# Performance work log

Measured on AMD Instinct MI355X. Metric: run time of the kernel, lower is better.

The kernel has to match this reference:

```python
import jax, jax.numpy as jnp
import numpy as np

NUM_HEADS = 12

def _get_rel_pos(q_size, k_size, rel_pos):
    # rel_pos already has shape (2*max(q,k)-1, head_dim) -> no resize needed
    q_coords = jnp.arange(q_size)[:, None] * max(k_size / q_size, 1.0)
    k_coords = jnp.arange(k_size)[None, :] * max(q_size / k_size, 1.0)
    rel = (q_coords - k_coords + (k_size - 1) * max(q_size / k_size, 1.0)).astype(jnp.int32)
    return rel_pos[rel.reshape(-1)].reshape(q_size, k_size, -1)  # (q, k, head_dim)


def setup_inputs() -> dict:
    key = jax.random.key(0)
    ks = jax.random.split(key, 7)
    B, H, W, C = 1, 64, 64, 768
    head_dim = C // NUM_HEADS
    return {
        "x": jax.random.normal(ks[0], (B, H, W, C), jnp.float32),
        "qkv_w": jax.random.normal(ks[1], (C, 3 * C), jnp.float32) * 0.02,
        "qkv_b": jax.random.normal(ks[2], (3 * C,), jnp.float32) * 0.02,
        "rel_pos_h": jax.random.normal(ks[3], (2 * H - 1, head_dim), jnp.float32) * 0.02,
        "rel_pos_w": jax.random.normal(ks[4], (2 * W - 1, head_dim), jnp.float32) * 0.02,
        "proj_w": jax.random.normal(ks[5], (C, C), jnp.float32) * 0.02,
        "proj_b": jax.random.normal(ks[6], (C,), jnp.float32) * 0.02,
    }


def reference(x, qkv_w, qkv_b, rel_pos_h, rel_pos_w, proj_w, proj_b):
    B, H, W, C = x.shape
    nh = NUM_HEADS
    hd = C // nh
    scale = hd ** (-0.5)
    S = H * W

    qkv = x @ qkv_w + qkv_b                              # (B,H,W,3C)
    qkv = qkv.reshape(B, S, 3, nh, hd).transpose(2, 0, 3, 1, 4).reshape(3, B * nh, S, hd)
    q, k, v = qkv[0], qkv[1], qkv[2]                     # (B*nh, S, hd)

    attn = jnp.einsum('bqd,bkd->bqk', q * scale, k)      # (B*nh, S, S)

    rh = _get_rel_pos(H, H, rel_pos_h)                   # (H,H,hd)
    rw = _get_rel_pos(W, W, rel_pos_w)                   # (W,W,hd)
    r_q = q.reshape(B * nh, H, W, hd)
    rel_h = jnp.einsum('bhwc,hkc->bhwk', r_q, rh)        # (B*nh,H,W,H)
    rel_w = jnp.einsum('bhwc,wkc->bhwk', r_q, rw)        # (B*nh,H,W,W)
    attn = (attn.reshape(B * nh, H, W, H, W)
            + rel_h[:, :, :, :, None]
            + rel_w[:, :, :, None, :]).reshape(B * nh, S, S)

    attn = jax.nn.softmax(attn, axis=-1)
    out = jnp.einsum('bqk,bkd->bqd', attn, v)            # (B*nh, S, hd)
    out = out.reshape(B, nh, H, W, hd).transpose(0, 2, 3, 1, 4).reshape(B, H, W, C)
    return out @ proj_w + proj_b
```

## Files before the change

kernel.cpp:

```cpp
#include <hip/hip_runtime.h>
#include <hip/hip_bf16.h>

#define S_TOK 4096
#define CDIM  768
#define N3C   2304
#define NH    12
#define HD    64

#define LOG2E 1.44269504f

typedef __attribute__((ext_vector_type(8))) short short8;
typedef __attribute__((ext_vector_type(4))) short short4v;
typedef __attribute__((ext_vector_type(4))) float float4v;
typedef __attribute__((ext_vector_type(4))) unsigned uint4v;

__device__ __forceinline__ float b2f(short s) {
    return __uint_as_float(((unsigned)(unsigned short)s) << 16);
}
__device__ __forceinline__ short f2b(float f) {
    unsigned u = __float_as_uint(f);
    unsigned r = (u + 0x7FFFu + ((u >> 16) & 1u)) >> 16;
    return (short)r;
}

#if __has_builtin(__builtin_amdgcn_exp2f)
#define EXP2F __builtin_amdgcn_exp2f
#else
#define EXP2F exp2f
#endif

__device__ __forceinline__ unsigned pack_trunc(float a, float b) {
    return __builtin_amdgcn_perm(__float_as_uint(b), __float_as_uint(a), 0x07060302u);
}

__device__ __forceinline__ short8 u4_to_s8(unsigned a, unsigned b, unsigned c, unsigned d) {
    union { uint4v u; short8 s; } t;
    t.u = (uint4v){a, b, c, d};
    return t.s;
}

__device__ __forceinline__ void load_lds16(const void* g, void* l) {
    __builtin_amdgcn_global_load_lds(
        (const __attribute__((address_space(1))) unsigned int*)g,
        (__attribute__((address_space(3))) unsigned int*)l, 16, 0, 0);
}

__global__ __launch_bounds__(256) void prep_kernel(
    const float* __restrict__ x, const float* __restrict__ qkvw,
    const float* __restrict__ pw,
    short* __restrict__ xb, short* __restrict__ wt, short* __restrict__ pwt)
{
    __shared__ float t[64][65];
    const int bid = blockIdx.x;
    const int tid = threadIdx.x;

    if (bid < 576) {
        const float* in;
        short* out;
        int C, bx, by;
        if (bid < 432) { in = qkvw; out = wt;  C = N3C;  bx = bid % 36;  by = bid / 36; }
        else           { in = pw;   out = pwt; C = CDIM; bx = (bid - 432) % 12; by = (bid - 432) / 12; }
        const int c0 = bx * 64, r0 = by * 64;
        const int li = tid >> 6;
        const int lj = tid & 63;
#pragma unroll
        for (int p = 0; p < 16; ++p) {
            int i = p * 4 + li;
            t[i][lj] = in[(size_t)(r0 + i) * C + c0 + lj];
        }
        __syncthreads();
#pragma unroll
        for (int p = 0; p < 16; ++p) {
            int i = p * 4 + li;
            out[(size_t)(c0 + i) * CDIM + r0 + lj] = f2b(t[lj][i]);
        }
    } else {
        const int i = (bid - 576) * 256 + tid;
        float4 v = ((const float4*)x)[i];
        short4v o4 = { f2b(v.x), f2b(v.y), f2b(v.z), f2b(v.w) };
        *(short4v*)&xb[(size_t)i * 4] = o4;
    }
}

#define GEMM_CORE(A_, Bt_, m0_, n0_)                                           \
    __shared__ __align__(16) short smem[2][128][64];                           \
    auto a_s = smem[0];                                                        \
    auto b_s = smem[1];                                                        \
    const int tid  = threadIdx.x;                                              \
    const int m0 = (m0_);                                                      \
    const int n0 = (n0_);                                                      \
    const int lane = tid & 63, w = tid >> 6;                                   \
    const int l15 = lane & 15, quad = lane >> 4;                               \
    const int wr = w >> 1, wc = w & 1;                                         \
    const int roff0 = (quad ^ (l15 & 7)) << 4;                                 \
    const int roff1 = roff0 ^ 64;                                              \
    const int srow0 = w * 8 + (lane >> 3);                                     \
    const int sslot = (lane & 7) ^ ((lane >> 3) & 7);                          \
    const short* ga = A_ + (size_t)(m0 + srow0) * 768 + sslot * 8;             \
    const short* gb = Bt_ + (size_t)(n0 + srow0) * 768 + sslot * 8;            \
    short* la = &a_s[w * 8][0];                                                \
    short* lb = &b_s[w * 8][0];                                                \
    float4v acc[4][4];                                                         \
    _Pragma("unroll")                                                          \
    for (int i = 0; i < 4; ++i)                                                \
        _Pragma("unroll")                                                      \
        for (int j = 0; j < 4; ++j) acc[i][j] = (float4v){0.f,0.f,0.f,0.f};    \
    for (int k0 = 0; k0 < 768; k0 += 64) {                                     \
        __syncthreads();                                                       \
        _Pragma("unroll")                                                      \
        for (int i = 0; i < 4; ++i) {                                          \
            load_lds16(ga + (size_t)i * (32 * 768) + k0, la + i * 32 * 64);    \
            load_lds16(gb + (size_t)i * (32 * 768) + k0, lb + i * 32 * 64);    \
        }                                                                      \
        __syncthreads();                                                       \
        _Pragma("unroll")                                                      \
        for (int kk = 0; kk < 64; kk += 32) {                                  \
            const int roff = kk ? roff1 : roff0;                               \
            short8 af[4], bfr[4];                                              \
            _Pragma("unroll")                                                  \
            for (int i = 0; i < 4; ++i)                                        \
                af[i] = *(const short8*)((const char*)&a_s[wr*64 + i*16 + l15][0] + roff); \
            _Pragma("unroll")                                                  \
            for (int j = 0; j < 4; ++j)                                        \
                bfr[j] = *(const short8*)((const char*)&b_s[wc*64 + j*16 + l15][0] + roff); \
            _Pragma("unroll")                                                  \
            for (int i = 0; i < 4; ++i)                                        \
                _Pragma("unroll")                                              \
                for (int j = 0; j < 4; ++j)                                    \
                    acc[i][j] = __builtin_amdgcn_mfma_f32_16x16x32_bf16(       \
                        af[i], bfr[j], acc[i][j], 0, 0, 0);                    \
        }                                                                      \
    }

__global__ __launch_bounds__(256) void gemm_qkv_mfma(
    const short* __restrict__ A, const short* __restrict__ Bt,
    const float* __restrict__ bias,
    short* __restrict__ Qb, short* __restrict__ Kb, short* __restrict__ Vt)
{
    const int flat = blockIdx.x;
    const int logi = (flat & 7) * 72 + (flat >> 3);
    GEMM_CORE(A, Bt, (logi / 18) * 128, (logi % 18) * 128)

    const int sec = n0 / CDIM;
    float bj[4];
#pragma unroll
    for (int j = 0; j < 4; ++j) bj[j] = bias[n0 + wc*64 + j*16 + l15];

    if (sec < 2) {
        short* base = (sec == 0) ? Qb : Kb;
        short (*tile)[68] = (short(*)[68])&smem[0][0][0];
#pragma unroll
        for (int h = 0; h < 2; ++h) {
            __syncthreads();
            if (wc == h) {
#pragma unroll
                for (int i = 0; i < 4; ++i)
#pragma unroll
                    for (int j = 0; j < 4; ++j)
#pragma unroll
                        for (int r = 0; r < 4; ++r)
                            tile[wr*64 + i*16 + quad*4 + r][j*16 + l15] =
                                f2b(acc[i][j][r] + bj[j]);
            }
            __syncthreads();
            const int nn = (n0 % CDIM) + h * 64;
            const int head = nn >> 6;
            short* dst = base + ((size_t)head * S_TOK + m0) * HD;
#pragma unroll
            for (int it = 0; it < 4; ++it) {
                const int row = it * 32 + (tid >> 3), c = (tid & 7) * 8;
                *(short8*)&dst[(size_t)row * HD + c] = *(const short8*)&tile[row][c];
            }
        }
    } else {
        short (*tv)[130] = (short(*)[130])&smem[0][0][0];
#pragma unroll
        for (int h = 0; h < 2; ++h) {
            __syncthreads();
            if (wc == h) {
#pragma unroll
                for (int i = 0; i < 4; ++i)
#pragma unroll
                    for (int j = 0; j < 4; ++j) {
                        short4v v4;
#pragma unroll
                        for (int r = 0; r < 4; ++r) v4[r] = f2b(acc[i][j][r] + bj[j]);
                        *(short4v*)&tv[j*16 + l15][wr*64 + i*16 + quad*4] = v4;
                    }
            }
            __syncthreads();
            const int nn = (n0 % CDIM) + h * 64;
            const int head = nn >> 6;
            short* dst = Vt + (size_t)head * HD * S_TOK + m0;
#pragma unroll
            for (int it = 0; it < 4; ++it) {
                const int nr = it * 16 + (tid >> 4), sc = (tid & 15) * 8;
                *(short8*)&dst[(size_t)nr * S_TOK + sc] = *(const short8*)&tv[nr][sc];
            }
        }
    }
}

__global__ __launch_bounds__(256) void gemm_proj_mfma(
    const short* __restrict__ A, const short* __restrict__ Bt,
    const float* __restrict__ bias, float* __restrict__ out)
{
    const int flat = blockIdx.x;
    const int logi = (flat & 7) * 24 + (flat >> 3);
    GEMM_CORE(A, Bt, (logi / 6) * 128, (logi % 6) * 128)

    float bj[4];
#pragma unroll
    for (int j = 0; j < 4; ++j) bj[j] = bias[n0 + wc*64 + j*16 + l15];

    float* tf = (float*)&smem[0][0][0];
#pragma unroll
    for (int h = 0; h < 2; ++h) {
        __syncthreads();
        if (wr == h) {
#pragma unroll
            for (int i = 0; i < 4; ++i)
#pragma unroll
                for (int j = 0; j < 4; ++j) {
                    const int cc = wc*16 + j*4 + (l15 >> 2);
                    const int ci = l15 & 3;
#pragma unroll
                    for (int r = 0; r < 4; ++r) {
                        const int row = i*16 + quad*4 + r;
                        const int pc = cc ^ ((row & 7) << 2);
                        tf[row * 128 + pc * 4 + ci] = acc[i][j][r] + bj[j];
                    }
                }
        }
        __syncthreads();
        float* dst = out + (size_t)(m0 + h * 64) * CDIM + n0;
#pragma unroll
        for (int it = 0; it < 8; ++it) {
            const int row = it * 8 + (tid >> 5);
            const int gc = tid & 31;
            const int pc = gc ^ ((row & 7) << 2);
            float4 v = *(const float4*)&tf[row * 128 + pc * 4];
            *(float4*)&dst[(size_t)row * CDIM + gc * 4] = v;
        }
    }
}

__global__ __launch_bounds__(256) void rel_mfma_kernel(
    const short* __restrict__ Qb, const float* __restrict__ rph,
    const float* __restrict__ rpw, short* __restrict__ RelhT,
    short* __restrict__ Relw)
{
    __shared__ __align__(16) short q_s [64][72];
    __shared__ __align__(16) short rh_s[64][72];
    __shared__ __align__(16) short rw_s[128][72];
    __shared__ __align__(16) short relw_t[64][64];

    const int tid  = threadIdx.x;
    const int y    = blockIdx.x;
    const int head = blockIdx.y;
    const int s0   = y * 64;
    const int w = tid >> 6, lane = tid & 63;
    const int l15 = lane & 15, quad = lane >> 4;
    const int srow = tid >> 2;
    const int scol = (tid & 3) << 4;

    {
        const uint4* g = (const uint4*)(Qb + ((size_t)head * S_TOK + s0 + srow) * HD + scol);
        *(uint4*)&q_s[srow][scol]     = g[0];
        *(uint4*)&q_s[srow][scol + 8] = g[1];
    }
    {
        const float* g = rph + (size_t)(y + srow) * HD + scol;
        short tmp[16];
#pragma unroll
        for (int i = 0; i < 16; i += 4) {
            float4 v = *(const float4*)(g + i);
            tmp[i] = f2b(v.x); tmp[i+1] = f2b(v.y); tmp[i+2] = f2b(v.z); tmp[i+3] = f2b(v.w);
        }
        *(short8*)&rh_s[srow][scol]     = *(short8*)&tmp[0];
        *(short8*)&rh_s[srow][scol + 8] = *(short8*)&tmp[8];
    }
#pragma unroll
    for (int half = 0; half < 2; ++half) {
        const int row = srow + half * 64;
        const int rr  = row > 126 ? 126 : row;
        const float* g = rpw + (size_t)rr * HD + scol;
        short tmp[16];
#pragma unroll
        for (int i = 0; i < 16; i += 4) {
            float4 v = *(const float4*)(g + i);
            tmp[i] = f2b(v.x); tmp[i+1] = f2b(v.y); tmp[i+2] = f2b(v.z); tmp[i+3] = f2b(v.w);
        }
        *(short8*)&rw_s[row][scol]     = *(short8*)&tmp[0];
        *(short8*)&rw_s[row][scol + 8] = *(short8*)&tmp[8];
    }
    __syncthreads();

    const short8 qa0 = *(const short8*)&q_s[w * 16 + l15][quad * 8];
    const short8 qa1 = *(const short8*)&q_s[w * 16 + l15][32 + quad * 8];

#pragma unroll
    for (int ct = 0; ct < 4; ++ct) {
        const int jj = ct * 16 + l15;
        short8 b0 = *(const short8*)&rh_s[jj][quad * 8];
        short8 b1 = *(const short8*)&rh_s[jj][32 + quad * 8];
        float4v z = (float4v){0.f, 0.f, 0.f, 0.f};
        z = __builtin_amdgcn_mfma_f32_16x16x32_bf16(qa0, b0, z, 0, 0, 0);
        z = __builtin_amdgcn_mfma_f32_16x16x32_bf16(qa1, b1, z, 0, 0, 0);
        const int ky = 63 - jj;
        short4v o4;
#pragma unroll
        for (int r = 0; r < 4; ++r) o4[r] = f2b(z[r] * LOG2E);
        *(short4v*)&RelhT[((size_t)head * HD + ky) * S_TOK + s0 + w * 16 + quad * 4] = o4;
    }

#pragma unroll
    for (int ct = 0; ct < 8; ++ct) {
        const int j = ct * 16 + l15;
        short8 b0 = *(const short8*)&rw_s[j][quad * 8];
        short8 b1 = *(const short8*)&rw_s[j][32 + quad * 8];
        float4v z = (float4v){0.f, 0.f, 0.f, 0.f};
        z = __builtin_amdgcn_mfma_f32_16x16x32_bf16(qa0, b0, z, 0, 0, 0);
        z = __builtin_amdgcn_mfma_f32_16x16x32_bf16(qa1, b1, z, 0, 0, 0);
#pragma unroll
        for (int r = 0; r < 4; ++r) {
            const int q  = w * 16 + quad * 4 + r;
            const int kx = q + 63 - j;
            if (kx >= 0 && kx < 64)
                relw_t[q][kx] = f2b(z[r] * LOG2E);
        }
    }
    __syncthreads();
    {
        const int row = tid >> 2, c = (tid & 3) * 16;
        short* dst = Relw + ((size_t)head * S_TOK + s0 + row) * HD + c;
        *(short8*)(dst)     = *(const short8*)&relw_t[row][c];
        *(short8*)(dst + 8) = *(const short8*)&relw_t[row][c + 8];
    }
}

__global__ __launch_bounds__(256, 3) void flash_kernel(
    const short* __restrict__ Qb, const short* __restrict__ Kb,
    const short* __restrict__ Vt, const short* __restrict__ RelhT,
    const short* __restrict__ Relw, short* __restrict__ attn_b)
{
    __shared__ __align__(16) short lds_s[24576];

    const int tid  = threadIdx.x;
    const int bid  = blockIdx.x;
    const int logi = (bid & 7) * 96 + (bid >> 3);
    const int head = logi >> 6;
    const int s0   = (logi & 63) << 6;
    const int w    = tid >> 6, lane = tid & 63;
    const int l15  = lane & 15, quad = lane >> 4;
    const int ph   = w >> 1;
    const int qh   = w & 1;

    const float C1 = 0.125f * LOG2E;

    const int lj = lane >> 3;
    const int sl = (lane & 7) ^ lj;
    const int kf0 = (lj & 3) + ((lj & 4) << 1) + qh * 32;

    const short* pKs = Kb + (size_t)head * S_TOK * HD
                     + (size_t)(ph * 32 * 64 + kf0) * HD + sl * 8;
    const short* pVs = Vt + ((size_t)head * HD + qh * 32 + lj) * S_TOK
                     + ph * 32 * 64 + sl * 8;

    short* lk0 = &lds_s[(ph * 2 + 0) << 12] + qh * 32 * 64;
    short* lk1 = &lds_s[(ph * 2 + 1) << 12] + qh * 32 * 64;
    short* lv  = &lds_s[16384 + (ph << 12)] + qh * 32 * 64;
    const short* krd0 = &lds_s[(ph * 2 + 0) << 12];
    const short* krd1 = &lds_s[(ph * 2 + 1) << 12];
    const short* vrd  = &lds_s[16384 + (ph << 12)];

    const int roff0 = (quad ^ (l15 & 7)) << 4;
    const int roff1 = roff0 ^ 64;

    short8 qb[2][2];
#pragma unroll
    for (int qt = 0; qt < 2; ++qt) {
        const short* qrow = Qb + ((size_t)head * S_TOK + s0 + qh * 32 + qt * 16 + l15) * HD;
        qb[qt][0] = *(const short8*)(qrow + quad * 8);
        qb[qt][1] = *(const short8*)(qrow + 32 + quad * 8);
    }

    float rwv[2][4][4];
#pragma unroll
    for (int qt = 0; qt < 2; ++qt) {
        const short* rwrow = Relw + ((size_t)head * S_TOK + s0 + qh * 32 + qt * 16 + l15) * HD;
#pragma unroll
        for (int kt = 0; kt < 4; ++kt) {
            const int base = ((kt & 1) << 2) | ((kt >> 1) << 5);
            short4v v = *(const short4v*)(rwrow + base + quad * 8);
#pragma unroll
            for (int r = 0; r < 4; ++r) rwv[qt][kt][r] = b2f(v[r]);
        }
    }

    const short* rhbase = RelhT + (size_t)head * HD * S_TOK + s0 + qh * 32 + l15;
    float rhc0 = b2f(rhbase[(size_t)(ph * 32) * S_TOK]);
    float rhc1 = b2f(rhbase[(size_t)(ph * 32) * S_TOK + 16]);

    short8 aones;
#pragma unroll
    for (int j = 0; j < 8; ++j) aones[j] = (short)0x3F80;

    float4v od[2][4];
#pragma unroll
    for (int qt = 0; qt < 2; ++qt)
#pragma unroll
        for (int dt = 0; dt < 4; ++dt) od[qt][dt] = (float4v){0.f, 0.f, 0.f, 0.f};
    float4v dq0 = (float4v){0.f, 0.f, 0.f, 0.f};
    float4v dq1 = (float4v){0.f, 0.f, 0.f, 0.f};

    load_lds16(pKs,        lk0);
    load_lds16(pKs + 1024, lk0 + 8  * 64);
    load_lds16(pKs + 256,  lk0 + 16 * 64);
    load_lds16(pKs + 1280, lk0 + 24 * 64);
    __syncthreads();

#define S_PHASE(krd_)                                                          \
        unsigned pkk[2][8];                                                    \
        _Pragma("unroll")                                                      \
        for (int kt = 0; kt < 4; ++kt) {                                       \
            const char* krp = (const char*)((krd_) + (kt * 16 + l15) * 64);    \
            const short8 ka0 = *(const short8*)(krp + roff0);                  \
            const short8 ka1 = *(const short8*)(krp + roff1);                  \
            {                                                                  \
                float4v z = (float4v){0.f, 0.f, 0.f, 0.f};                     \
                z = __builtin_amdgcn_mfma_f32_16x16x32_bf16(ka0, qb[0][0], z, 0, 0, 0); \
                z = __builtin_amdgcn_mfma_f32_16x16x32_bf16(ka1, qb[0][1], z, 0, 0, 0); \
                float p0 = EXP2F(C1 * z[0] + (rhc0 + rwv[0][kt][0]));          \
                float p1 = EXP2F(C1 * z[1] + (rhc0 + rwv[0][kt][1]));          \
                float p2 = EXP2F(C1 * z[2] + (rhc0 + rwv[0][kt][2]));          \
                float p3 = EXP2F(C1 * z[3] + (rhc0 + rwv[0][kt][3]));          \
                pkk[0][kt * 2]     = pack_trunc(p0, p1);                       \
                pkk[0][kt * 2 + 1] = pack_trunc(p2, p3);                       \
            }                                                                  \
            {                                                                  \
                float4v z = (float4v){0.f, 0.f, 0.f, 0.f};                     \
                z = __builtin_amdgcn_mfma_f32_16x16x32_bf16(ka0, qb[1][0], z, 0, 0, 0); \
                z = __builtin_amdgcn_mfma_f32_16x16x32_bf16(ka1, qb[1][1], z, 0, 0, 0); \
                float p0 = EXP2F(C1 * z[0] + (rhc1 + rwv[1][kt][0]));          \
                float p1 = EXP2F(C1 * z[1] + (rhc1 + rwv[1][kt][1]));          \
                float p2 = EXP2F(C1 * z[2] + (rhc1 + rwv[1][kt][2]));          \
                float p3 = EXP2F(C1 * z[3] + (rhc1 + rwv[1][kt][3]));          \
                pkk[1][kt * 2]     = pack_trunc(p0, p1);                       \
                pkk[1][kt * 2 + 1] = pack_trunc(p2, p3);                       \
            }                                                                  \
        }                                                                      \
        const short8 pb00 = u4_to_s8(pkk[0][0], pkk[0][1], pkk[0][2], pkk[0][3]); \
        const short8 pb01 = u4_to_s8(pkk[0][4], pkk[0][5], pkk[0][6], pkk[0][7]); \
        const short8 pb10 = u4_to_s8(pkk[1][0], pkk[1][1], pkk[1][2], pkk[1][3]); \
        const short8 pb11 = u4_to_s8(pkk[1][4], pkk[1][5], pkk[1][6], pkk[1][7]);

#define PV_PHASE                                                               \
        __builtin_amdgcn_s_setprio(1);                                         \
        _Pragma("unroll")                                                      \
        for (int dt = 0; dt < 4; ++dt) {                                       \
            const char* vrp = (const char*)(vrd + (dt * 16 + l15) * 64);       \
            const short8 va0 = *(const short8*)(vrp + roff0);                  \
            const short8 va1 = *(const short8*)(vrp + roff1);                  \
            od[0][dt] = __builtin_amdgcn_mfma_f32_16x16x32_bf16(va0, pb00, od[0][dt], 0, 0, 0); \
            od[0][dt] = __builtin_amdgcn_mfma_f32_16x16x32_bf16(va1, pb01, od[0][dt], 0, 0, 0); \
            od[1][dt] = __builtin_amdgcn_mfma_f32_16x16x32_bf16(va0, pb10, od[1][dt], 0, 0, 0); \
            od[1][dt] = __builtin_amdgcn_mfma_f32_16x16x32_bf16(va1, pb11, od[1][dt], 0, 0, 0); \
        }                                                                      \
        dq0 = __builtin_amdgcn_mfma_f32_16x16x32_bf16(aones, pb00, dq0, 0, 0, 0); \
        dq0 = __builtin_amdgcn_mfma_f32_16x16x32_bf16(aones, pb01, dq0, 0, 0, 0); \
        dq1 = __builtin_amdgcn_mfma_f32_16x16x32_bf16(aones, pb10, dq1, 0, 0, 0); \
        dq1 = __builtin_amdgcn_mfma_f32_16x16x32_bf16(aones, pb11, dq1, 0, 0, 0); \
        __builtin_amdgcn_s_setprio(0);

    for (int t = 0; t < 31; ++t) {
        const int cur = t & 1;
        const short* krd = cur ? krd1 : krd0;
        short* lkn = cur ? lk0 : lk1;

        load_lds16(pVs,               lv);
        load_lds16(pVs + 8  * S_TOK,  lv + 8  * 64);
        load_lds16(pVs + 16 * S_TOK,  lv + 16 * 64);
        load_lds16(pVs + 24 * S_TOK,  lv + 24 * 64);
        asm volatile("" ::: "memory");
        short rhn0 = rhbase[(size_t)(ph * 32 + t + 1) * S_TOK];
        short rhn1 = rhbase[(size_t)(ph * 32 + t + 1) * S_TOK + 16];
        asm volatile("" ::: "memory");
        {
            const short* pk = pKs + 4096;
            load_lds16(pk,        lkn);
            load_lds16(pk + 1024, lkn + 8  * 64);
            load_lds16(pk + 256,  lkn + 16 * 64);
            load_lds16(pk + 1280, lkn + 24 * 64);
        }
        pKs += 4096;
        pVs += 64;

        asm volatile("s_waitcnt vmcnt(10)" ::: "memory");
        __builtin_amdgcn_sched_barrier(0);
        __builtin_amdgcn_s_barrier();

        S_PHASE(krd)

        asm volatile("s_waitcnt vmcnt(6)" ::: "memory");
        __builtin_amdgcn_sched_barrier(0);
        __builtin_amdgcn_s_barrier();

        PV_PHASE

        rhc0 = b2f(rhn0);
        rhc1 = b2f(rhn1);

        __builtin_amdgcn_s_barrier();
    }

    {
        const short* krd = krd1;
        load_lds16(pVs,               lv);
        load_lds16(pVs + 8  * S_TOK,  lv + 8  * 64);
        load_lds16(pVs + 16 * S_TOK,  lv + 16 * 64);
        load_lds16(pVs + 24 * S_TOK,  lv + 24 * 64);

        asm volatile("s_waitcnt vmcnt(4)" ::: "memory");
        __builtin_amdgcn_sched_barrier(0);
        __builtin_amdgcn_s_barrier();

        S_PHASE(krd)

        asm volatile("s_waitcnt vmcnt(0)" ::: "memory");
        __builtin_amdgcn_sched_barrier(0);
        __builtin_amdgcn_s_barrier();

        PV_PHASE
    }
#undef S_PHASE
#undef PV_PHASE

    float* cf = (float*)lds_s;
    if (ph == 1) {
#pragma unroll
        for (int qt = 0; qt < 2; ++qt)
#pragma unroll
            for (int dt = 0; dt < 4; ++dt) {
                float* dst = &cf[((((qh * 2 + qt) * 4 + dt) * 16) + quad * 4) * 16 + l15];
#pragma unroll
                for (int r = 0; r < 4; ++r) dst[r * 16] = od[qt][dt][r];
            }
        if (quad == 0) {
            cf[4096 + (qh * 2 + 0) * 16 + l15] = dq0[0];
            cf[4096 + (qh * 2 + 1) * 16 + l15] = dq1[0];
        }
    }
    __syncthreads();
    if (ph == 0) {
#pragma unroll
        for (int qt = 0; qt < 2; ++qt) {
            const float dtot = ((qt == 0) ? dq0[0] : dq1[0])
                             + cf[4096 + (qh * 2 + qt) * 16 + l15];
            const float inv = 1.f / dtot;
            short* outp = attn_b + (size_t)(s0 + qh * 32 + qt * 16 + l15) * CDIM + head * HD;
#pragma unroll
            for (int dt = 0; dt < 4; ++dt) {
                const float* src = &cf[((((qh * 2 + qt) * 4 + dt) * 16) + quad * 4) * 16 + l15];
                short4v o4;
#pragma unroll
                for (int r = 0; r < 4; ++r)
                    o4[r] = f2b((od[qt][dt][r] + src[r * 16]) * inv);
                *(short4v*)(outp + dt * 16 + quad * 4) = o4;
            }
        }
    }
}

extern "C" void kernel_launch(void* const* d_in, const int* in_sizes, int n_in,
                              void* d_out, int out_size, void* d_ws, size_t ws_size,
                              hipStream_t stream)
{
    const float* x    = (const float*)d_in[0];
    const float* qkvw = (const float*)d_in[1];
    const float* qkvb = (const float*)d_in[2];
    const float* rph  = (const float*)d_in[3];
    const float* rpw  = (const float*)d_in[4];
    const float* pw   = (const float*)d_in[5];
    const float* pb   = (const float*)d_in[6];
    float* out = (float*)d_out;

    const size_t HSD = (size_t)NH * S_TOK * HD;
    short* xb     = (short*)d_ws;
    short* wt     = xb + (size_t)S_TOK * CDIM;
    short* pwt    = wt + (size_t)N3C * CDIM;
    short* Qb     = pwt + (size_t)CDIM * CDIM;
    short* Kb     = Qb + HSD;
    short* Vt     = Kb + HSD;
    short* RelhT  = Vt + HSD;
    short* Relw   = RelhT + HSD;
    short* attn_b = Relw + HSD;

    prep_kernel<<<dim3(576 + S_TOK * CDIM / 4 / 256), 256, 0, stream>>>(
        x, qkvw, pw, xb, wt, pwt);

    gemm_qkv_mfma<<<dim3((N3C / 128) * (S_TOK / 128)), 256, 0, stream>>>(
        xb, wt, qkvb, Qb, Kb, Vt);
    rel_mfma_kernel<<<dim3(64, NH), 256, 0, stream>>>(Qb, rph, rpw, RelhT, Relw);
    flash_kernel<<<dim3(64 * NH), 256, 0, stream>>>(Qb, Kb, Vt, RelhT, Relw, attn_b);
    gemm_proj_mfma<<<dim3((CDIM / 128) * (S_TOK / 128)), 256, 0, stream>>>(
        attn_b, pwt, pb, out);
}
```

Measured before the change: 204.5 us.

## Double-buffer LDS tiles in GEMM core to overlap global loads with MFMA

```diff
diff --git a/kernel.cpp b/kernel.cpp
--- a/kernel.cpp
+++ b/kernel.cpp
@@ -82,10 +82,36 @@
     }
 }
 
+#define GSTAGE(k0_, bb_)                                                       \
+        _Pragma("unroll")                                                      \
+        for (int i = 0; i < 4; ++i) {                                          \
+            load_lds16(ga + (size_t)i * (32 * 768) + (k0_),                    \
+                       &smem[bb_][w * 8 + i * 32][0]);                         \
+            load_lds16(gb + (size_t)i * (32 * 768) + (k0_),                    \
+                       &smem[(bb_) + 1][w * 8 + i * 32][0]);                   \
+        }
+
+#define GCOMPUTE(bb_)                                                          \
+        _Pragma("unroll")                                                      \
+        for (int kk = 0; kk < 64; kk += 32) {                                  \
+            const int roff = kk ? roff1 : roff0;                               \
+            short8 af[4], bfr[4];                                              \
+            _Pragma("unroll")                                                  \
+            for (int i = 0; i < 4; ++i)                                        \
+                af[i] = *(const short8*)((const char*)&smem[bb_][wr*64 + i*16 + l15][0] + roff); \
+            _Pragma("unroll")                                                  \
+            for (int j = 0; j < 4; ++j)                                        \
+                bfr[j] = *(const short8*)((const char*)&smem[(bb_)+1][wc*64 + j*16 + l15][0] + roff); \
+            _Pragma("unroll")                                                  \
+            for (int i = 0; i < 4; ++i)                                        \
+                _Pragma("unroll")                                              \
+                for (int j = 0; j < 4; ++j)                                    \
+                    acc[i][j] = __builtin_amdgcn_mfma_f32_16x16x32_bf16(       \
+                        af[i], bfr[j], acc[i][j], 0, 0, 0);                    \
+        }
+
 #define GEMM_CORE(A_, Bt_, m0_, n0_)                                           \
-    __shared__ __align__(16) short smem[2][128][64];                           \
-    auto a_s = smem[0];                                                        \
-    auto b_s = smem[1];                                                        \
+    __shared__ __align__(16) short smem[4][128][64];                           \
     const int tid  = threadIdx.x;                                              \
     const int m0 = (m0_);                                                      \
     const int n0 = (n0_);                                                      \
@@ -98,38 +124,32 @@
     const int sslot = (lane & 7) ^ ((lane >> 3) & 7);                          \
     const short* ga = A_ + (size_t)(m0 + srow0) * 768 + sslot * 8;             \
     const short* gb = Bt_ + (size_t)(n0 + srow0) * 768 + sslot * 8;            \
-    short* la = &a_s[w * 8][0];                                                \
-    short* lb = &b_s[w * 8][0];                                                \
     float4v acc[4][4];                                                         \
     _Pragma("unroll")                                                          \
     for (int i = 0; i < 4; ++i)                                                \
         _Pragma("unroll")                                                      \
         for (int j = 0; j < 4; ++j) acc[i][j] = (float4v){0.f,0.f,0.f,0.f};    \
-    for (int k0 = 0; k0 < 768; k0 += 64) {                                     \
-        __syncthreads();                                                       \
-        _Pragma("unroll")                                                      \
-        for (int i = 0; i < 4; ++i) {                                          \
-            load_lds16(ga + (size_t)i * (32 * 768) + k0, la + i * 32 * 64);    \
-            load_lds16(gb + (size_t)i * (32 * 768) + k0, lb + i * 32 * 64);    \
+    GSTAGE(0, 0)                                                               \
+    _Pragma("unroll")                                                          \
+    for (int tp = 0; tp < 6; ++tp) {                                           \
+              \
+        GSTAGE(tp * 128 + 64, 2)                                               \
+        asm volatile("s_waitcnt vmcnt(8)" ::: "memory");                       \
+        __builtin_amdgcn_sched_barrier(0);                                     \
+        __builtin_amdgcn_s_barrier();                                          \
+        GCOMPUTE(0)                                                            \
+        __builtin_amdgcn_s_barrier();                                          \
+                 \
+        if (tp < 5) {                                                          \
+            GSTAGE(tp * 128 + 128, 0)                                          \
+            asm volatile("s_waitcnt vmcnt(8)" ::: "memory");                   \
+        } else {                                                               \
+            asm volatile("s_waitcnt vmcnt(0)" ::: "memory");                   \
         }                                                                      \
-        __syncthreads();                                                       \
-        _Pragma("unroll")                                                      \
-        for (int kk = 0; kk < 64; kk += 32) {                                  \
-            const int roff = kk ? roff1 : roff0;                               \
-            short8 af[4], bfr[4];                                              \
-            _Pragma("unroll")                                                  \
-            for (int i = 0; i < 4; ++i)                                        \
-                af[i] = *(const short8*)((const char*)&a_s[wr*64 + i*16 + l15][0] + roff); \
-            _Pragma("unroll")                                                  \
-            for (int j = 0; j < 4; ++j)                                        \
-                bfr[j] = *(const short8*)((const char*)&b_s[wc*64 + j*16 + l15][0] + roff); \
-            _Pragma("unroll")                                                  \
-            for (int i = 0; i < 4; ++i)                                        \
-                _Pragma("unroll")                                              \
-                for (int j = 0; j < 4; ++j)                                    \
-                    acc[i][j] = __builtin_amdgcn_mfma_f32_16x16x32_bf16(       \
-                        af[i], bfr[j], acc[i][j], 0, 0, 0);                    \
-        }                                                                      \
+        __builtin_amdgcn_sched_barrier(0);                                     \
+        __builtin_amdgcn_s_barrier();                                          \
+        GCOMPUTE(2)                                                            \
+        __builtin_amdgcn_s_barrier();                                          \
     }
 
 __global__ __launch_bounds__(256) void gemm_qkv_mfma(
```

Result: faster. 190.5 us (-6.8%).
